# Optimization experiments

Hardware: AMD Instinct MI355X
Metric: run time of the kernel (lower is better)

Reference implementation:

```python
import jax, jax.numpy as jnp
import numpy as np

K = 8          # num groups
SIZE = 250     # state/hidden size (h1 = h2 = 250)
M = 576        # flattened input size (24x24)
B = 2048       # batch
HA = 100       # attention hidden
EPS = 1e-5


def _ln(x, g, b):
    mu = jnp.mean(x, axis=-1, keepdims=True)
    v = jnp.mean(jnp.square(x - mu), axis=-1, keepdims=True)
    return (x - mu) * jax.lax.rsqrt(v + EPS) * g + b


def setup_inputs() -> dict:
    key = jax.random.key(0)
    ks = jax.random.split(key, 10)
    def w(k, shape):
        return jax.random.normal(k, shape, jnp.float32) / np.sqrt(shape[0]).astype(np.float32)
    inp = {
        "x": jax.random.normal(ks[0], (B * K, M), jnp.float32),
        "state": jax.random.normal(ks[1], (B * K, SIZE), jnp.float32),
        # encoder: Linear(SIZE,250) + ReLU + LN(250)
        "enc_W": w(ks[2], (SIZE, 250)), "enc_b": jnp.zeros((250,), jnp.float32),
        "enc_g": jnp.ones((250,), jnp.float32), "enc_bt": jnp.zeros((250,), jnp.float32),
        # core: Linear(500,250) + ReLU + LN(250)
        "core_W": w(ks[3], (500, 250)), "core_b": jnp.zeros((250,), jnp.float32),
        "core_g": jnp.ones((250,), jnp.float32), "core_bt": jnp.zeros((250,), jnp.float32),
        # context: Linear(250,250) + ReLU + LN(250)
        "ctx_W": w(ks[4], (250, 250)), "ctx_b": jnp.zeros((250,), jnp.float32),
        "ctx_g": jnp.ones((250,), jnp.float32), "ctx_bt": jnp.zeros((250,), jnp.float32),
        # attention: Linear(250,100)+Tanh+LN(100)+Linear(100,1)+Sigmoid
        "att_W1": w(ks[5], (250, HA)), "att_b1": jnp.zeros((HA,), jnp.float32),
        "att_g": jnp.ones((HA,), jnp.float32), "att_bt": jnp.zeros((HA,), jnp.float32),
        "att_W2": w(ks[6], (HA, 1)), "att_b2": jnp.zeros((1,), jnp.float32),
        # output: Linear(250 + 250 + M, SIZE)
        "out_W": w(ks[7], (250 + 250 + M, SIZE)), "out_b": jnp.zeros((SIZE,), jnp.float32),
    }
    return inp


def reference(x, state, enc_W, enc_b, enc_g, enc_bt, core_W, core_b, core_g, core_bt,
              ctx_W, ctx_b, ctx_g, ctx_bt, att_W1, att_b1, att_g, att_bt,
              att_W2, att_b2, out_W, out_b):
    bk = state.shape[0]
    b = bk // K
    h1 = 250
    # 0-1. encode state -> [B*K, h1]
    s1 = _ln(jax.nn.relu(state @ enc_W + enc_b), enc_g, enc_bt)
    s1r = s1.reshape(b, K, h1)
    # 2-3. focus / context pairs via static gather index [K, K-1]
    idx = np.array([[j for j in range(K) if j != i] for i in range(K)], np.int32)
    cs = s1r[:, idx]                                    # [b, K, K-1, h1]
    fs = jnp.broadcast_to(s1r[:, :, None, :], cs.shape)  # [b, K, K-1, h1]
    # 4. concat pairs -> [b*K*(K-1), 2*h1]
    concat = jnp.concatenate([fs, cs], axis=-1).reshape(b * K * (K - 1), 2 * h1)
    # 5. core MLP
    core_out = _ln(jax.nn.relu(concat @ core_W + core_b), core_g, core_bt)
    # context MLP
    context_out = _ln(jax.nn.relu(core_out @ ctx_W + ctx_b), ctx_g, ctx_bt)
    # attention scalar per pair
    att_h = _ln(jnp.tanh(core_out @ att_W1 + att_b1), att_g, att_bt)
    att = jax.nn.sigmoid(att_h @ att_W2 + att_b2)        # [b*K*(K-1), 1]
    # 6-7. attention-weighted sum over K-1 context effects -> [B*K, h2]
    effect_sum = jnp.sum(context_out.reshape(bk, K - 1, h1) * att.reshape(bk, K - 1, 1), axis=1)
    # 8. decode
    total = jnp.concatenate([s1, effect_sum, x], axis=1)  # [B*K, h1+h2+M]
    new_state = total @ out_W + out_b                     # [B*K, SIZE]
    return new_state
```

## Files before the change

kernel.cpp:

```cpp
#include <hip/hip_runtime.h>
#include <math.h>

#define KK 8
#define H 250
#define MDIM 576
#define NB 2048
#define HA 100
#define ROWS (NB*KK)
#define PQS 512
#define KP 1088
#define EFS 258
#define EPS 1e-5f

typedef unsigned short ushort_t;
typedef short short8 __attribute__((ext_vector_type(8)));
typedef unsigned short us8 __attribute__((ext_vector_type(8)));
typedef unsigned short us4 __attribute__((ext_vector_type(4)));
typedef unsigned short us2 __attribute__((ext_vector_type(2)));
typedef float f32x4 __attribute__((ext_vector_type(4)));

template<int CTRL>
__device__ __forceinline__ float dpp_add_f32(float x) {
    const int s = __builtin_amdgcn_update_dpp(
        0, __builtin_bit_cast(int, x), CTRL, 0xF, 0xF, true);
    return x + __builtin_bit_cast(float, s);
}
__device__ __forceinline__ float wave_sum_dpp(float x) {
    x = dpp_add_f32<0x111>(x);
    x = dpp_add_f32<0x112>(x);
    x = dpp_add_f32<0x114>(x);
    x = dpp_add_f32<0x118>(x);
    x = dpp_add_f32<0x142>(x);
    x = dpp_add_f32<0x143>(x);
    return __builtin_bit_cast(float, __builtin_amdgcn_readlane(
        __builtin_bit_cast(int, x), 63));
}
__device__ __forceinline__ float bfly16_sum(float x) {
    x = dpp_add_f32<0xB1>(x);
    x = dpp_add_f32<0x4E>(x);
    x = dpp_add_f32<0x141>(x);
    x = dpp_add_f32<0x140>(x);
    return x;
}

__device__ __forceinline__ void async_copy16(const void* g, void* l) {
    __builtin_amdgcn_global_load_lds(
        (const __attribute__((address_space(1))) void*)g,
        (__attribute__((address_space(3))) void*)l, 16, 0, 0);
}

__device__ __forceinline__ ushort_t f2bf(float v) {
    union { float f; unsigned int u; } c; c.f = v;
    unsigned int x = c.u;
    x += 0x7fff + ((x >> 16) & 1);
    return (ushort_t)(x >> 16);
}
__device__ __forceinline__ float bf2f(ushort_t v) {
    union { unsigned int u; float f; } c; c.u = ((unsigned int)v) << 16;
    return c.f;
}
__device__ __forceinline__ float ftanh(float x) {
    const float e = __expf(2.f * x);
    return 1.f - 2.f * __builtin_amdgcn_rcpf(e + 1.f);
}
__device__ __forceinline__ float fsigmoid(float x) {
    return __builtin_amdgcn_rcpf(1.f + __expf(-x));
}

__global__ __launch_bounds__(256) void k_prep(
    const float* __restrict__ out_W, const float* __restrict__ core_W,
    const float* __restrict__ ctx_W, const float* __restrict__ att_W1,
    const float* __restrict__ enc_W, const float* __restrict__ state,
    const float* __restrict__ x,
    ushort_t* __restrict__ Wt, ushort_t* __restrict__ Wpq,
    ushort_t* __restrict__ Wca, ushort_t* __restrict__ Wenc,
    ushort_t* __restrict__ Sb, ushort_t* __restrict__ Abuf)
{
    const int b = blockIdx.x, t = threadIdx.x;
    if (b < 256) {
        const int n = b;
        for (int k = t; k < KP; k += 256) {
            const float v = (n < H && k < 1076) ? out_W[(size_t)k * H + n] : 0.f;
            Wt[(size_t)n * KP + k] = f2bf(v);
        }
    } else if (b < 768) {
        const int n = b - 256, k = t;
        float v = 0.f;
        if (k < H) {
            if (n < H)                    v = core_W[(size_t)k * H + n];
            else if (n >= 256 && n < 506) v = core_W[(size_t)(H + k) * H + (n - 256)];
        }
        Wpq[(size_t)n * 256 + k] = f2bf(v);
    } else if (b < 1152) {
        const int n = b - 768, k = t;
        float v = 0.f;
        if (k < H) {
            if (n < H)           v = ctx_W[(size_t)k * H + n];
            else if (n < H + HA) v = att_W1[(size_t)k * HA + (n - H)];
        }
        Wca[(size_t)n * 256 + k] = f2bf(v);
    } else if (b < 1408) {
        const int n = b - 1152, k = t;
        const float v = (n < H && k < H) ? enc_W[(size_t)k * H + n] : 0.f;
        Wenc[(size_t)n * 256 + k] = f2bf(v);
    } else if (b < 2432) {
        const int r0 = (b - 1408) * 16;
        for (int idx = t; idx < 16 * 256; idx += 256) {
            const int r = r0 + (idx >> 8), k = idx & 255;
            const float v = (k < H) ? state[(size_t)r * H + k] : 0.f;
            Sb[(size_t)r * 256 + k] = f2bf(v);
        }
    } else {
        const int row = b - 2432;
        for (int c = 500 + t; c < KP; c += 256) {
            const float v = (c < 500 + MDIM) ? x[(size_t)row * MDIM + (c - 500)] : 0.f;
            Abuf[(size_t)row * KP + c] = f2bf(v);
        }
    }
}

template<int NT>
__global__ __launch_bounds__(512, NT == 8 ? 2 : 4) void k_gemm_nres(
    const ushort_t* __restrict__ A, int lda,
    const ushort_t* __restrict__ B, int ldb,
    void* __restrict__ Cp, int ldc,
    const float* __restrict__ bias,
    int ksteps, int nlim, int bf16out)
{
    constexpr int NROWS = NT * 64;
    __shared__ __align__(16) ushort_t As[64 * 32];
    __shared__ __align__(16) ushort_t Bs[NROWS * 32];
    const int tid = threadIdx.x, lane = tid & 63, wave = tid >> 6;
    const int wm = wave >> 2, wn = wave & 3;
    const int R0 = (int)blockIdx.x * 64;

    const int ar = tid >> 2, acb = tid & 3;
    const bool aon = tid < 256;
    const int acl = acb ^ ((ar >> 1) & 3);
    const ushort_t* gA = A + (size_t)(R0 + ar) * lda + acl * 8;

    const int q = lane >> 4, fr = lane & 15;

    f32x4 acc[2][NT] = {};
    for (int ks = 0; ks < ksteps; ++ks) {
        const int k0 = ks * 32;
        if (aon) async_copy16(gA + k0, &As[tid * 8]);
#pragma unroll
        for (int it = 0; it < NT / 2; ++it) {
            const int ci  = it * 512 + tid;
            const int rb  = ci >> 2, cb2 = ci & 3;
            const int clb = cb2 ^ ((rb >> 1) & 3);
            async_copy16(B + (size_t)rb * ldb + k0 + clb * 8, &Bs[ci * 8]);
        }
        __syncthreads();
        short8 a[2];
#pragma unroll
        for (int ms = 0; ms < 2; ++ms) {
            const int row = wm * 32 + ms * 16 + fr;
            a[ms] = *(const short8*)&As[(row * 4 + (q ^ ((row >> 1) & 3))) * 8];
        }
#pragma unroll
        for (int nt = 0; nt < NT; ++nt) {
            const int n = wn * (NT * 16) + nt * 16 + fr;
            const short8 b = *(const short8*)&Bs[(n * 4 + (q ^ ((n >> 1) & 3))) * 8];
#pragma unroll
            for (int ms = 0; ms < 2; ++ms)
                acc[ms][nt] = __builtin_amdgcn_mfma_f32_16x16x32_bf16(
                    a[ms], b, acc[ms][nt], 0, 0, 0);
        }
        __syncthreads();
    }

#pragma unroll
    for (int ms = 0; ms < 2; ++ms)
#pragma unroll
        for (int nt = 0; nt < NT; ++nt) {
            const int col = wn * (NT * 16) + nt * 16 + fr;
            if (col >= nlim) continue;
            const float bv = bias ? bias[col] : 0.f;
#pragma unroll
            for (int reg = 0; reg < 4; ++reg) {
                const int row = R0 + wm * 32 + ms * 16 + q * 4 + reg;
                const float v = acc[ms][nt][reg] + bv;
                if (bf16out) ((ushort_t*)Cp)[(size_t)row * ldc + col] = f2bf(v);
                else         ((float*)Cp)[(size_t)row * ldc + col] = v;
            }
        }
}

__global__ __launch_bounds__(256) void k_lnenc(const ushort_t* __restrict__ Epre,
    const float* __restrict__ eb, const float* __restrict__ eg,
    const float* __restrict__ ebt, ushort_t* __restrict__ Abuf)
{
    const int wave = threadIdx.x >> 6, lane = threadIdx.x & 63;
    const int row = blockIdx.x * 4 + wave;
    const int c0 = 4 * lane;

    const us4 v = *(const us4*)&Epre[(size_t)row * 256 + c0];
    float y[4]; float sm = 0.f, sq = 0.f;
#pragma unroll
    for (int t = 0; t < 4; ++t) {
        const int cc = c0 + t;
        float z = 0.f;
        if (cc < H) z = fmaxf(bf2f(v[t]) + eb[cc], 0.f);
        y[t] = z; sm += z; sq += z * z;
    }
    sm = wave_sum_dpp(sm);
    sq = wave_sum_dpp(sq);
    const float mu = sm * (1.f / H);
    const float rs = __builtin_amdgcn_rsqf(sq * (1.f / H) - mu * mu + EPS);
    ushort_t o[4];
#pragma unroll
    for (int t = 0; t < 4; ++t) {
        const int cc = c0 + t;
        o[t] = (cc < H) ? f2bf((y[t] - mu) * rs * eg[cc] + ebt[cc]) : (ushort_t)0;
    }
    ushort_t* dst = Abuf + (size_t)row * KP + c0;
    if (c0 + 3 < H) { *(us4*)dst = (us4){o[0], o[1], o[2], o[3]}; }
    else {
        if (c0 + 1 < H) *(us2*)dst = (us2){o[0], o[1]};
    }
}

__global__ __launch_bounds__(512, 2) void k_fuse(
    const ushort_t* __restrict__ PQb,
    const ushort_t* __restrict__ Wca,
    const float* __restrict__ core_b, const float* __restrict__ core_g,
    const float* __restrict__ core_bt,
    const float* __restrict__ ctx_b, const float* __restrict__ ctx_g,
    const float* __restrict__ ctx_bt,
    const float* __restrict__ att_b1, const float* __restrict__ att_g,
    const float* __restrict__ att_bt,
    const float* __restrict__ attW2, const float* __restrict__ att_b2,
    ushort_t* __restrict__ Abuf)
{
    __shared__ __align__(16) ushort_t As[32 * 256];
    __shared__ __align__(16) ushort_t Bs[384 * 32];
    __shared__ __align__(16) float red[32][36];
    __shared__ __align__(16) float effacc[32 * EFS];
    __shared__ float scal[32];
    __shared__ float sS0[32], sS1[32];
    __shared__ float swred[4][2];

    const int tid = threadIdx.x, lane = tid & 63, wave = tid >> 6;
    const int wm = wave >> 2, wn = wave & 3;
    const int q = lane >> 4, fr = lane & 15;
    const int g0 = (int)blockIdx.x * 32;

    bool eC[6], eA[6];
    float b_[6], gw[6];
    float psgw = 0.f, psbw = 0.f;
#pragma unroll
    for (int nt = 0; nt < 6; ++nt) {
        const int col = wn * 96 + nt * 16 + fr;
        eC[nt] = col < H;
        eA[nt] = (col >= H) && (col < H + HA);
        if (eC[nt]) {
            b_[nt] = ctx_b[col]; gw[nt] = 0.f;
        } else if (eA[nt]) {
            const int ca = col - H;
            b_[nt] = att_b1[ca];
            const float ga = att_g[ca], w2 = attW2[ca];
            gw[nt] = ga * w2;
            psgw += gw[nt]; psbw += att_bt[ca] * w2;
        } else {
            b_[nt] = gw[nt] = 0.f;
        }
    }
    psgw = bfly16_sum(psgw); psbw = bfly16_sum(psbw);
    if (lane == 0) { swred[wn][0] = psgw; swred[wn][1] = psbw; }
    for (int i = tid; i < 32 * EFS; i += 512) effacc[i] = 0.f;
    if (wave == 0 && lane < 32) { sS0[lane] = 0.f; sS1[lane] = 0.f; }
    __syncthreads();
    const float sgw = swred[0][0] + swred[1][0] + swred[2][0] + swred[3][0];
    const float ab2 = att_b2[0] +
        (swred[0][1] + swred[1][1] + swred[2][1] + swred[3][1]);

    const int cL = lane * 4;
    float cb4[4], cg4[4], cbt4[4]; bool vl4[4];
#pragma unroll
    for (int t = 0; t < 4; ++t) {
        vl4[t] = (cL + t) < H;
        cb4[t] = cg4[t] = cbt4[t] = 0.f;
        if (vl4[t]) { cb4[t] = core_b[cL + t]; cg4[t] = core_g[cL + t];
                      cbt4[t] = core_bt[cL + t]; }
    }

    const int arow = wm * 16 + fr;
    const int abase = arow * 256;
    const int arsw = arow & 7;

    for (int jj = 0; jj < 7; ++jj) {
#pragma unroll
        for (int pass = 0; pass < 4; ++pass) {
            const int r = pass * 8 + wave;
            const int ir = r & 7;
            const int j = jj + (jj >= ir ? 1 : 0);
            const us4 pu = *(const us4*)&PQb[(size_t)(g0 + r) * PQS + cL];
            const us4 qu = *(const us4*)&PQb[
                (size_t)(g0 + (r & ~7) + j) * PQS + 256 + cL];
            float z[4]; float sm = 0.f, sq = 0.f;
#pragma unroll
            for (int t = 0; t < 4; ++t) {
                float zz = 0.f;
                if (vl4[t]) zz = fmaxf(bf2f(pu[t]) + bf2f(qu[t]) + cb4[t], 0.f);
                z[t] = zz; sm += zz; sq = fmaf(zz, zz, sq);
            }
            sm = wave_sum_dpp(sm);
            sq = wave_sum_dpp(sq);
            const float mu = sm * (1.f / H);
            const float rs = __builtin_amdgcn_rsqf(sq * (1.f / H) - mu * mu + EPS);
            us4 o;
#pragma unroll
            for (int t = 0; t < 4; ++t)
                o[t] = vl4[t] ? f2bf((z[t] - mu) * rs * cg4[t] + cbt4[t])
                              : (ushort_t)0;
            const int p = (((lane >> 1) ^ (r & 7)) << 1) | (lane & 1);
            *(us4*)&As[r * 256 + p * 4] = o;
        }

        f32x4 acc[6] = {};
        for (int ks = 0; ks < 8; ++ks) {
#pragma unroll
            for (int it = 0; it < 3; ++it) {
                const int ci  = it * 512 + tid;
                const int rb  = ci >> 2, cb2 = ci & 3;
                const int clb = cb2 ^ ((rb >> 1) & 3);
                async_copy16(Wca + (size_t)rb * 256 + ks * 32 + clb * 8, &Bs[ci * 8]);
            }
            __syncthreads();
            const short8 a = *(const short8*)&As[abase + ((ks * 4 + q) ^ arsw) * 8];
#pragma unroll
            for (int nt = 0; nt < 6; ++nt) {
                const int n = wn * 96 + nt * 16 + fr;
                const short8 b = *(const short8*)&Bs[(n * 4 + (q ^ ((n >> 1) & 3))) * 8];
                acc[nt] = __builtin_amdgcn_mfma_f32_16x16x32_bf16(a, b, acc[nt], 0, 0, 0);
            }
            __syncthreads();
        }

        float smc[4] = {}, sqc[4] = {}, sma[4] = {}, sqa[4] = {}, szgw[4] = {};
#pragma unroll
        for (int nt = 0; nt < 6; ++nt) {
#pragma unroll
            for (int reg = 0; reg < 4; ++reg) {
                const float val = acc[nt][reg] + b_[nt];
                if (eC[nt]) {
                    const float zz = fmaxf(val, 0.f);
                    acc[nt][reg] = zz;
                    smc[reg] += zz; sqc[reg] = fmaf(zz, zz, sqc[reg]);
                } else if (eA[nt]) {
                    const float za = ftanh(val);
                    sma[reg] += za; sqa[reg] = fmaf(za, za, sqa[reg]);
                    szgw[reg] = fmaf(za, gw[nt], szgw[reg]);
                }
            }
        }
#pragma unroll
        for (int reg = 0; reg < 4; ++reg) {
            smc[reg]  = bfly16_sum(smc[reg]);
            sqc[reg]  = bfly16_sum(sqc[reg]);
            sma[reg]  = bfly16_sum(sma[reg]);
            sqa[reg]  = bfly16_sum(sqa[reg]);
            szgw[reg] = bfly16_sum(szgw[reg]);
        }
        if (fr == 0) {
#pragma unroll
            for (int reg = 0; reg < 4; ++reg) {
                const int row = wm * 16 + q * 4 + reg;
                *(f32x4*)&red[row][wn * 8] =
                    (f32x4){smc[reg], sqc[reg], sma[reg], sqa[reg]};
                red[row][wn * 8 + 4] = szgw[reg];
            }
        }
        __syncthreads();
        if (wave == 0 && lane < 32) {
            const int rr = lane;
            float s0 = 0.f, s1 = 0.f, s2 = 0.f, s3 = 0.f, s4 = 0.f;
#pragma unroll
            for (int w2 = 0; w2 < 4; ++w2) {
                const f32x4 v = *(const f32x4*)&red[rr][w2 * 8];
                s0 += v[0]; s1 += v[1]; s2 += v[2]; s3 += v[3];
                s4 += red[rr][w2 * 8 + 4];
            }
            const float muC = s0 * (1.f / H);
            const float rsC = __builtin_amdgcn_rsqf(s1 * (1.f / H) - muC * muC + EPS);
            const float muA = s2 * (1.f / HA);
            const float rsA = __builtin_amdgcn_rsqf(s3 * (1.f / HA) - muA * muA + EPS);
            const float dot = rsA * (s4 - muA * sgw) + ab2;
            const float ag  = fsigmoid(dot);
            const float cj  = ag * rsC;
            scal[rr] = cj;
            sS0[rr] += ag;
            sS1[rr] = fmaf(cj, muC, sS1[rr]);
        }
        __syncthreads();
#pragma unroll
        for (int reg = 0; reg < 4; ++reg) {
            const int row = wm * 16 + q * 4 + reg;
            const float cj = scal[row];
#pragma unroll
            for (int nt = 0; nt < 6; ++nt) {
                if (!eC[nt]) continue;
                const int col = wn * 96 + nt * 16 + fr;
                const int idx = row * EFS + col;
                effacc[idx] = fmaf(cj, acc[nt][reg], effacc[idx]);
            }
        }
    }

#pragma unroll
    for (int nt = 0; nt < 6; ++nt) {
        const int col = wn * 96 + nt * 16 + fr;
        if (col >= H) continue;
        const float gc = ctx_g[col], bc = ctx_bt[col];
#pragma unroll
        for (int reg = 0; reg < 4; ++reg) {
            const int row = wm * 16 + q * 4 + reg;
            const float a4 = effacc[row * EFS + col];
            const float o = gc * (a4 - sS1[row]) + bc * sS0[row];
            Abuf[(size_t)(g0 + row) * KP + H + col] = f2bf(o);
        }
    }
}

extern "C" void kernel_launch(void* const* d_in, const int* in_sizes, int n_in,
                              void* d_out, int out_size, void* d_ws, size_t ws_size,
                              hipStream_t stream)
{
    const float* x      = (const float*)d_in[0];
    const float* state  = (const float*)d_in[1];
    const float* enc_W  = (const float*)d_in[2];
    const float* enc_b  = (const float*)d_in[3];
    const float* enc_g  = (const float*)d_in[4];
    const float* enc_bt = (const float*)d_in[5];
    const float* core_W = (const float*)d_in[6];
    const float* core_b = (const float*)d_in[7];
    const float* core_g = (const float*)d_in[8];
    const float* core_bt= (const float*)d_in[9];
    const float* ctx_W  = (const float*)d_in[10];
    const float* ctx_b  = (const float*)d_in[11];
    const float* ctx_g  = (const float*)d_in[12];
    const float* ctx_bt = (const float*)d_in[13];
    const float* att_W1 = (const float*)d_in[14];
    const float* att_b1 = (const float*)d_in[15];
    const float* att_g  = (const float*)d_in[16];
    const float* att_bt = (const float*)d_in[17];
    const float* att_W2 = (const float*)d_in[18];
    const float* att_b2 = (const float*)d_in[19];
    const float* out_W  = (const float*)d_in[20];
    const float* out_b  = (const float*)d_in[21];
    float* out = (float*)d_out;

    ushort_t* Abuf = (ushort_t*)d_ws;
    ushort_t* Wt   = Abuf + (size_t)ROWS * KP;
    ushort_t* Wpq  = Wt + (size_t)256 * KP;
    ushort_t* Wca  = Wpq + (size_t)512 * 256;
    ushort_t* Wenc = Wca + (size_t)384 * 256;
    ushort_t* Sb   = Wenc + (size_t)256 * 256;
    ushort_t* Epre = Sb + (size_t)ROWS * 256;
    ushort_t* PQb  = Epre + (size_t)ROWS * 256;

    k_prep  <<<2432 + ROWS, 256, 0, stream>>>(out_W, core_W, ctx_W, att_W1, enc_W,
                                              state, x, Wt, Wpq, Wca, Wenc, Sb, Abuf);
    k_gemm_nres<4><<<ROWS / 64, 512, 0, stream>>>(Sb, 256, Wenc, 256, Epre, 256,
                                                  nullptr, 8, 256, 1);
    k_lnenc <<<ROWS / 4, 256, 0, stream>>>(Epre, enc_b, enc_g, enc_bt, Abuf);
    k_gemm_nres<8><<<ROWS / 64, 512, 0, stream>>>(Abuf, KP, Wpq, 256, PQb, PQS,
                                                  nullptr, 8, 512, 1);
    k_fuse  <<<ROWS / 32, 512, 0, stream>>>(PQb, Wca,
                                            core_b, core_g, core_bt,
                                            ctx_b, ctx_g, ctx_bt,
                                            att_b1, att_g, att_bt,
                                            att_W2, att_b2, Abuf);
    k_gemm_nres<4><<<ROWS / 64, 512, 0, stream>>>(Abuf, KP, Wt, KP, out, H,
                                                  out_b, KP / 32, 250, 0);
}
```

Measured before the change: 348.2 us.

## Batch four pair-slices per weight load and keep effect sum in registers

The seven sequential j-iterations are regrouped into two sweeps of four and three slices. Each sweep builds a 128-row A tile in LDS, and every B-tile fetch of the combined context/attention weights is reused across up to four MFMA row-groups. That cuts weight reloads and block barriers per slice. The attention-weighted effect accumulator moves from an LDS array into registers, removing the LDS read-modify-write traffic and the zero-fill. The costs are a larger As buffer in LDS (128x256 bf16) and about 96 accumulator registers per lane, which could lower occupancy under the 512x2 launch bound.

```diff
diff --git a/kernel.cpp b/kernel.cpp
--- a/kernel.cpp
+++ b/kernel.cpp
@@ -9,7 +9,6 @@
 #define ROWS (NB*KK)
 #define PQS 512
 #define KP 1088
-#define EFS 258
 #define EPS 1e-5f
 
 typedef unsigned short ushort_t;
@@ -234,10 +233,9 @@
     const float* __restrict__ attW2, const float* __restrict__ att_b2,
     ushort_t* __restrict__ Abuf)
 {
-    __shared__ __align__(16) ushort_t As[32 * 256];
+    __shared__ __align__(16) ushort_t As[128 * 256];
     __shared__ __align__(16) ushort_t Bs[384 * 32];
     __shared__ __align__(16) float red[32][36];
-    __shared__ __align__(16) float effacc[32 * EFS];
     __shared__ float scal[32];
     __shared__ float sS0[32], sS1[32];
     __shared__ float swred[4][2];
@@ -269,7 +267,6 @@
     }
     psgw = bfly16_sum(psgw); psbw = bfly16_sum(psbw);
     if (lane == 0) { swred[wn][0] = psgw; swred[wn][1] = psbw; }
-    for (int i = tid; i < 32 * EFS; i += 512) effacc[i] = 0.f;
     if (wave == 0 && lane < 32) { sS0[lane] = 0.f; sS1[lane] = 0.f; }
     __syncthreads();
     const float sgw = swred[0][0] + swred[1][0] + swred[2][0] + swred[3][0];
@@ -287,18 +284,23 @@
     }
 
     const int arow = wm * 16 + fr;
-    const int abase = arow * 256;
     const int arsw = arow & 7;
 
-    for (int jj = 0; jj < 7; ++jj) {
-#pragma unroll
-        for (int pass = 0; pass < 4; ++pass) {
-            const int r = pass * 8 + wave;
-            const int ir = r & 7;
-            const int j = jj + (jj >= ir ? 1 : 0);
-            const us4 pu = *(const us4*)&PQb[(size_t)(g0 + r) * PQS + cL];
+    f32x4 A4[6] = {};
+
+    for (int sw = 0; sw < 2; ++sw) {
+        const int jb = sw * 4;
+        const int nj = 4 - sw;
+
+        for (int pass = 0; pass < nj * 4; ++pass) {
+            const int gr = pass * 8 + wave;
+            const int rl = gr & 31;
+            const int jj = jb + (gr >> 5);
+            const int ir = rl & 7;
+            const int j  = jj + (jj >= ir ? 1 : 0);
+            const us4 pu = *(const us4*)&PQb[(size_t)(g0 + rl) * PQS + cL];
             const us4 qu = *(const us4*)&PQb[
-                (size_t)(g0 + (r & ~7) + j) * PQS + 256 + cL];
+                (size_t)(g0 + (rl & ~7) + j) * PQS + 256 + cL];
             float z[4]; float sm = 0.f, sq = 0.f;
 #pragma unroll
             for (int t = 0; t < 4; ++t) {
@@ -315,11 +317,11 @@
             for (int t = 0; t < 4; ++t)
                 o[t] = vl4[t] ? f2bf((z[t] - mu) * rs * cg4[t] + cbt4[t])
                               : (ushort_t)0;
-            const int p = (((lane >> 1) ^ (r & 7)) << 1) | (lane & 1);
-            *(us4*)&As[r * 256 + p * 4] = o;
-        }
-
-        f32x4 acc[6] = {};
+            const int p = (((lane >> 1) ^ (rl & 7)) << 1) | (lane & 1);
+            *(us4*)&As[gr * 256 + p * 4] = o;
+        }
+
+        f32x4 acc[4][6] = {};
         for (int ks = 0; ks < 8; ++ks) {
 #pragma unroll
             for (int it = 0; it < 3; ++it) {
@@ -329,82 +331,93 @@
                 async_copy16(Wca + (size_t)rb * 256 + ks * 32 + clb * 8, &Bs[ci * 8]);
             }
             __syncthreads();
-            const short8 a = *(const short8*)&As[abase + ((ks * 4 + q) ^ arsw) * 8];
+            short8 bfr[6];
 #pragma unroll
             for (int nt = 0; nt < 6; ++nt) {
                 const int n = wn * 96 + nt * 16 + fr;
-                const short8 b = *(const short8*)&Bs[(n * 4 + (q ^ ((n >> 1) & 3))) * 8];
-                acc[nt] = __builtin_amdgcn_mfma_f32_16x16x32_bf16(a, b, acc[nt], 0, 0, 0);
+                bfr[nt] = *(const short8*)&Bs[(n * 4 + (q ^ ((n >> 1) & 3))) * 8];
+            }
+#pragma unroll
+            for (int u = 0; u < 4; ++u) {
+                if (u < nj) {
+                    const short8 a = *(const short8*)&As[
+                        (u * 32 + arow) * 256 + ((ks * 4 + q) ^ arsw) * 8];
+#pragma unroll
+                    for (int nt = 0; nt < 6; ++nt)
+                        acc[u][nt] = __builtin_amdgcn_mfma_f32_16x16x32_bf16(
+                            a, bfr[nt], acc[u][nt], 0, 0, 0);
+                }
             }
             __syncthreads();
         }
 
-        float smc[4] = {}, sqc[4] = {}, sma[4] = {}, sqa[4] = {}, szgw[4] = {};
-#pragma unroll
-        for (int nt = 0; nt < 6; ++nt) {
+#pragma unroll
+        for (int u = 0; u < 4; ++u) {
+            if (u >= nj) continue;
+            float smc[4] = {}, sqc[4] = {}, sma[4] = {}, sqa[4] = {}, szgw[4] = {};
+#pragma unroll
+            for (int nt = 0; nt < 6; ++nt) {
+#pragma unroll
+                for (int reg = 0; reg < 4; ++reg) {
+                    const float val = acc[u][nt][reg] + b_[nt];
+                    if (eC[nt]) {
+                        const float zz = fmaxf(val, 0.f);
+                        acc[u][nt][reg] = zz;
+                        smc[reg] += zz; sqc[reg] = fmaf(zz, zz, sqc[reg]);
+                    } else if (eA[nt]) {
+                        const float za = ftanh(val);
+                        sma[reg] += za; sqa[reg] = fmaf(za, za, sqa[reg]);
+                        szgw[reg] = fmaf(za, gw[nt], szgw[reg]);
+                    }
+                }
+            }
 #pragma unroll
             for (int reg = 0; reg < 4; ++reg) {
-                const float val = acc[nt][reg] + b_[nt];
-                if (eC[nt]) {
-                    const float zz = fmaxf(val, 0.f);
-                    acc[nt][reg] = zz;
-                    smc[reg] += zz; sqc[reg] = fmaf(zz, zz, sqc[reg]);
-                } else if (eA[nt]) {
-                    const float za = ftanh(val);
-                    sma[reg] += za; sqa[reg] = fmaf(za, za, sqa[reg]);
-                    szgw[reg] = fmaf(za, gw[nt], szgw[reg]);
+                smc[reg]  = bfly16_sum(smc[reg]);
+                sqc[reg]  = bfly16_sum(sqc[reg]);
+                sma[reg]  = bfly16_sum(sma[reg]);
+                sqa[reg]  = bfly16_sum(sqa[reg]);
+                szgw[reg] = bfly16_sum(szgw[reg]);
+            }
+            if (fr == 0) {
+#pragma unroll
+                for (int reg = 0; reg < 4; ++reg) {
+                    const int row = wm * 16 + q * 4 + reg;
+                    *(f32x4*)&red[row][wn * 8] =
+                        (f32x4){smc[reg], sqc[reg], sma[reg], sqa[reg]};
+                    red[row][wn * 8 + 4] = szgw[reg];
                 }
             }
-        }
-#pragma unroll
-        for (int reg = 0; reg < 4; ++reg) {
-            smc[reg]  = bfly16_sum(smc[reg]);
-            sqc[reg]  = bfly16_sum(sqc[reg]);
-            sma[reg]  = bfly16_sum(sma[reg]);
-            sqa[reg]  = bfly16_sum(sqa[reg]);
-            szgw[reg] = bfly16_sum(szgw[reg]);
-        }
-        if (fr == 0) {
+            __syncthreads();
+            if (wave == 0 && lane < 32) {
+                const int rr = lane;
+                float s0 = 0.f, s1 = 0.f, s2 = 0.f, s3 = 0.f, s4 = 0.f;
+#pragma unroll
+                for (int w2 = 0; w2 < 4; ++w2) {
+                    const f32x4 v = *(const f32x4*)&red[rr][w2 * 8];
+                    s0 += v[0]; s1 += v[1]; s2 += v[2]; s3 += v[3];
+                    s4 += red[rr][w2 * 8 + 4];
+                }
+                const float muC = s0 * (1.f / H);
+                const float rsC = __builtin_amdgcn_rsqf(s1 * (1.f / H) - muC * muC + EPS);
+                const float muA = s2 * (1.f / HA);
+                const float rsA = __builtin_amdgcn_rsqf(s3 * (1.f / HA) - muA * muA + EPS);
+                const float dot = rsA * (s4 - muA * sgw) + ab2;
+                const float ag  = fsigmoid(dot);
+                const float cj  = ag * rsC;
+                scal[rr] = cj;
+                sS0[rr] += ag;
+                sS1[rr] = fmaf(cj, muC, sS1[rr]);
+            }
+            __syncthreads();
 #pragma unroll
             for (int reg = 0; reg < 4; ++reg) {
                 const int row = wm * 16 + q * 4 + reg;
-                *(f32x4*)&red[row][wn * 8] =
-                    (f32x4){smc[reg], sqc[reg], sma[reg], sqa[reg]};
-                red[row][wn * 8 + 4] = szgw[reg];
-            }
-        }
-        __syncthreads();
-        if (wave == 0 && lane < 32) {
-            const int rr = lane;
-            float s0 = 0.f, s1 = 0.f, s2 = 0.f, s3 = 0.f, s4 = 0.f;
-#pragma unroll
-            for (int w2 = 0; w2 < 4; ++w2) {
-                const f32x4 v = *(const f32x4*)&red[rr][w2 * 8];
-                s0 += v[0]; s1 += v[1]; s2 += v[2]; s3 += v[3];
-                s4 += red[rr][w2 * 8 + 4];
-            }
-            const float muC = s0 * (1.f / H);
-            const float rsC = __builtin_amdgcn_rsqf(s1 * (1.f / H) - muC * muC + EPS);
-            const float muA = s2 * (1.f / HA);
-            const float rsA = __builtin_amdgcn_rsqf(s3 * (1.f / HA) - muA * muA + EPS);
-            const float dot = rsA * (s4 - muA * sgw) + ab2;
-            const float ag  = fsigmoid(dot);
-            const float cj  = ag * rsC;
-            scal[rr] = cj;
-            sS0[rr] += ag;
-            sS1[rr] = fmaf(cj, muC, sS1[rr]);
-        }
-        __syncthreads();
-#pragma unroll
-        for (int reg = 0; reg < 4; ++reg) {
-            const int row = wm * 16 + q * 4 + reg;
-            const float cj = scal[row];
-#pragma unroll
-            for (int nt = 0; nt < 6; ++nt) {
-                if (!eC[nt]) continue;
-                const int col = wn * 96 + nt * 16 + fr;
-                const int idx = row * EFS + col;
-                effacc[idx] = fmaf(cj, acc[nt][reg], effacc[idx]);
+                const float cj = scal[row];
+#pragma unroll
+                for (int nt = 0; nt < 6; ++nt)
+                    if (eC[nt])
+                        A4[nt][reg] = fmaf(cj, acc[u][nt][reg], A4[nt][reg]);
             }
         }
     }
@@ -417,8 +430,7 @@
 #pragma unroll
         for (int reg = 0; reg < 4; ++reg) {
             const int row = wm * 16 + q * 4 + reg;
-            const float a4 = effacc[row * EFS + col];
-            const float o = gc * (a4 - sS1[row]) + bc * sS0[row];
+            const float o = gc * (A4[nt][reg] - sS1[row]) + bc * sS0[row];
             Abuf[(size_t)(g0 + row) * KP + H + col] = f2bf(o);
         }
     }
```

Result: faster. 322.6 us (-7.3%).

## Split fused core/context kernel into core-LN pass plus pair-tiled context GEMM

Applied to the files above, without the earlier changes.

The fused kernel, which recomputed the core LayerNorm per pair inside a 7-iteration loop with a 32-row GEMM, is split into two kernels. The first writes all core outputs (B*K*7 rows) to a workspace buffer in bf16. The second runs a 64-row-tiled GEMM over flattened pair rows, grouping 9 groups (63 rows) per block, and accumulates the attention-weighted effect sums with LDS atomics. This trades an extra global round trip of about 58 MB of intermediate for better MFMA tile utilisation, fewer weight reloads per row and higher occupancy.

```diff
diff --git a/kernel.cpp b/kernel.cpp
--- a/kernel.cpp
+++ b/kernel.cpp
@@ -7,9 +7,10 @@
 #define NB 2048
 #define HA 100
 #define ROWS (NB*KK)
+#define PROWS (ROWS*7)
 #define PQS 512
 #define KP 1088
-#define EFS 258
+#define NGB 9
 #define EPS 1e-5f
 
 typedef unsigned short ushort_t;
@@ -222,11 +223,63 @@
     }
 }
 
-__global__ __launch_bounds__(512, 2) void k_fuse(
-    const ushort_t* __restrict__ PQb,
+__global__ __launch_bounds__(256) void k_core(const ushort_t* __restrict__ PQb,
+    const float* __restrict__ core_b, const float* __restrict__ core_g,
+    const float* __restrict__ core_bt, ushort_t* __restrict__ Co)
+{
+    const int wave = threadIdx.x >> 6, lane = threadIdx.x & 63;
+    const int g = blockIdx.x * 4 + wave;
+    const int i = g & 7;
+    const int c = lane * 4;
+
+    const us4 pu = *(const us4*)&PQb[(size_t)g * PQS + c];
+    us4 qu[7];
+#pragma unroll
+    for (int jj = 0; jj < 7; ++jj) {
+        const int j = jj + (jj >= i ? 1 : 0);
+        const int qr = (g & ~7) + j;
+        qu[jj] = *(const us4*)&PQb[(size_t)qr * PQS + 256 + c];
+    }
+    float pe[4], cb[4], cg[4], cbt[4]; bool vl[4];
+#pragma unroll
+    for (int t = 0; t < 4; ++t) {
+        vl[t]  = (c + t) < H;
+        pe[t]  = bf2f(pu[t]);
+        cb[t]  = vl[t] ? core_b[c + t]  : 0.f;
+        cg[t]  = vl[t] ? core_g[c + t]  : 0.f;
+        cbt[t] = vl[t] ? core_bt[c + t] : 0.f;
+    }
+    float z[7][4], red[7][2];
+#pragma unroll
+    for (int jj = 0; jj < 7; ++jj) {
+        float sm = 0.f, sq = 0.f;
+#pragma unroll
+        for (int t = 0; t < 4; ++t) {
+            const float zz = vl[t] ? fmaxf(pe[t] + bf2f(qu[jj][t]) + cb[t], 0.f) : 0.f;
+            z[jj][t] = zz; sm += zz; sq = fmaf(zz, zz, sq);
+        }
+        red[jj][0] = sm; red[jj][1] = sq;
+    }
+#pragma unroll
+    for (int jj = 0; jj < 7; ++jj) {
+        red[jj][0] = wave_sum_dpp(red[jj][0]);
+        red[jj][1] = wave_sum_dpp(red[jj][1]);
+    }
+#pragma unroll
+    for (int jj = 0; jj < 7; ++jj) {
+        const float mu = red[jj][0] * (1.f / H);
+        const float rs = __builtin_amdgcn_rsqf(red[jj][1] * (1.f / H) - mu * mu + EPS);
+        us4 o;
+#pragma unroll
+        for (int t = 0; t < 4; ++t)
+            o[t] = vl[t] ? f2bf((z[jj][t] - mu) * rs * cg[t] + cbt[t]) : (ushort_t)0;
+        *(us4*)&Co[((size_t)g * 7 + jj) * 256 + c] = o;
+    }
+}
+
+__global__ __launch_bounds__(512, 4) void k_cseff(
+    const ushort_t* __restrict__ Co,
     const ushort_t* __restrict__ Wca,
-    const float* __restrict__ core_b, const float* __restrict__ core_g,
-    const float* __restrict__ core_bt,
     const float* __restrict__ ctx_b, const float* __restrict__ ctx_g,
     const float* __restrict__ ctx_bt,
     const float* __restrict__ att_b1, const float* __restrict__ att_g,
@@ -234,18 +287,59 @@
     const float* __restrict__ attW2, const float* __restrict__ att_b2,
     ushort_t* __restrict__ Abuf)
 {
-    __shared__ __align__(16) ushort_t As[32 * 256];
+    __shared__ __align__(16) ushort_t As[64 * 32];
     __shared__ __align__(16) ushort_t Bs[384 * 32];
-    __shared__ __align__(16) float red[32][36];
-    __shared__ __align__(16) float effacc[32 * EFS];
-    __shared__ float scal[32];
-    __shared__ float sS0[32], sS1[32];
+    __shared__ __align__(16) float red[64][36];
+    __shared__ __align__(16) float scal[64][4];
+    __shared__ __align__(16) float effacc[NGB * 252];
+    __shared__ float sS0[NGB], sS1[NGB];
     __shared__ float swred[4][2];
 
     const int tid = threadIdx.x, lane = tid & 63, wave = tid >> 6;
     const int wm = wave >> 2, wn = wave & 3;
     const int q = lane >> 4, fr = lane & 15;
-    const int g0 = (int)blockIdx.x * 32;
+    const int gb0 = (int)blockIdx.x * NGB;
+    const int ngroups = min(NGB, ROWS - gb0);
+    const int nrows = ngroups * 7;
+    const int R0r = gb0 * 7;
+
+    for (int i = tid; i < NGB * 252; i += 512) effacc[i] = 0.f;
+
+    const int ar = tid >> 2, acb = tid & 3;
+    const bool aon = tid < 256;
+    const int acl = acb ^ ((ar >> 1) & 3);
+    const int arr = (ar < nrows) ? ar : (nrows - 1);
+    const ushort_t* gA = Co + (size_t)(R0r + arr) * 256 + acl * 8;
+
+    f32x4 acc[2][6] = {};
+    for (int ks = 0; ks < 8; ++ks) {
+        const int k0 = ks * 32;
+        if (aon) async_copy16(gA + k0, &As[tid * 8]);
+#pragma unroll
+        for (int it = 0; it < 3; ++it) {
+            const int ci  = it * 512 + tid;
+            const int rb  = ci >> 2, cb2 = ci & 3;
+            const int clb = cb2 ^ ((rb >> 1) & 3);
+            async_copy16(Wca + (size_t)rb * 256 + k0 + clb * 8, &Bs[ci * 8]);
+        }
+        __syncthreads();
+        short8 a[2];
+#pragma unroll
+        for (int ms = 0; ms < 2; ++ms) {
+            const int row = wm * 32 + ms * 16 + fr;
+            a[ms] = *(const short8*)&As[(row * 4 + (q ^ ((row >> 1) & 3))) * 8];
+        }
+#pragma unroll
+        for (int nt = 0; nt < 6; ++nt) {
+            const int n = wn * 96 + nt * 16 + fr;
+            const short8 b = *(const short8*)&Bs[(n * 4 + (q ^ ((n >> 1) & 3))) * 8];
+#pragma unroll
+            for (int ms = 0; ms < 2; ++ms)
+                acc[ms][nt] = __builtin_amdgcn_mfma_f32_16x16x32_bf16(
+                    a[ms], b, acc[ms][nt], 0, 0, 0);
+        }
+        __syncthreads();
+    }
 
     bool eC[6], eA[6];
     float b_[6], gw[6];
@@ -255,99 +349,29 @@
         const int col = wn * 96 + nt * 16 + fr;
         eC[nt] = col < H;
         eA[nt] = (col >= H) && (col < H + HA);
-        if (eC[nt]) {
-            b_[nt] = ctx_b[col]; gw[nt] = 0.f;
-        } else if (eA[nt]) {
+        if (eC[nt]) { b_[nt] = ctx_b[col]; gw[nt] = 0.f; }
+        else if (eA[nt]) {
             const int ca = col - H;
             b_[nt] = att_b1[ca];
-            const float ga = att_g[ca], w2 = attW2[ca];
-            gw[nt] = ga * w2;
+            const float w2 = attW2[ca];
+            gw[nt] = att_g[ca] * w2;
             psgw += gw[nt]; psbw += att_bt[ca] * w2;
-        } else {
-            b_[nt] = gw[nt] = 0.f;
-        }
+        } else { b_[nt] = gw[nt] = 0.f; }
     }
     psgw = bfly16_sum(psgw); psbw = bfly16_sum(psbw);
     if (lane == 0) { swred[wn][0] = psgw; swred[wn][1] = psbw; }
-    for (int i = tid; i < 32 * EFS; i += 512) effacc[i] = 0.f;
-    if (wave == 0 && lane < 32) { sS0[lane] = 0.f; sS1[lane] = 0.f; }
-    __syncthreads();
-    const float sgw = swred[0][0] + swred[1][0] + swred[2][0] + swred[3][0];
-    const float ab2 = att_b2[0] +
-        (swred[0][1] + swred[1][1] + swred[2][1] + swred[3][1]);
-
-    const int cL = lane * 4;
-    float cb4[4], cg4[4], cbt4[4]; bool vl4[4];
-#pragma unroll
-    for (int t = 0; t < 4; ++t) {
-        vl4[t] = (cL + t) < H;
-        cb4[t] = cg4[t] = cbt4[t] = 0.f;
-        if (vl4[t]) { cb4[t] = core_b[cL + t]; cg4[t] = core_g[cL + t];
-                      cbt4[t] = core_bt[cL + t]; }
-    }
-
-    const int arow = wm * 16 + fr;
-    const int abase = arow * 256;
-    const int arsw = arow & 7;
-
-    for (int jj = 0; jj < 7; ++jj) {
-#pragma unroll
-        for (int pass = 0; pass < 4; ++pass) {
-            const int r = pass * 8 + wave;
-            const int ir = r & 7;
-            const int j = jj + (jj >= ir ? 1 : 0);
-            const us4 pu = *(const us4*)&PQb[(size_t)(g0 + r) * PQS + cL];
-            const us4 qu = *(const us4*)&PQb[
-                (size_t)(g0 + (r & ~7) + j) * PQS + 256 + cL];
-            float z[4]; float sm = 0.f, sq = 0.f;
-#pragma unroll
-            for (int t = 0; t < 4; ++t) {
-                float zz = 0.f;
-                if (vl4[t]) zz = fmaxf(bf2f(pu[t]) + bf2f(qu[t]) + cb4[t], 0.f);
-                z[t] = zz; sm += zz; sq = fmaf(zz, zz, sq);
-            }
-            sm = wave_sum_dpp(sm);
-            sq = wave_sum_dpp(sq);
-            const float mu = sm * (1.f / H);
-            const float rs = __builtin_amdgcn_rsqf(sq * (1.f / H) - mu * mu + EPS);
-            us4 o;
-#pragma unroll
-            for (int t = 0; t < 4; ++t)
-                o[t] = vl4[t] ? f2bf((z[t] - mu) * rs * cg4[t] + cbt4[t])
-                              : (ushort_t)0;
-            const int p = (((lane >> 1) ^ (r & 7)) << 1) | (lane & 1);
-            *(us4*)&As[r * 256 + p * 4] = o;
-        }
-
-        f32x4 acc[6] = {};
-        for (int ks = 0; ks < 8; ++ks) {
-#pragma unroll
-            for (int it = 0; it < 3; ++it) {
-                const int ci  = it * 512 + tid;
-                const int rb  = ci >> 2, cb2 = ci & 3;
-                const int clb = cb2 ^ ((rb >> 1) & 3);
-                async_copy16(Wca + (size_t)rb * 256 + ks * 32 + clb * 8, &Bs[ci * 8]);
-            }
-            __syncthreads();
-            const short8 a = *(const short8*)&As[abase + ((ks * 4 + q) ^ arsw) * 8];
-#pragma unroll
-            for (int nt = 0; nt < 6; ++nt) {
-                const int n = wn * 96 + nt * 16 + fr;
-                const short8 b = *(const short8*)&Bs[(n * 4 + (q ^ ((n >> 1) & 3))) * 8];
-                acc[nt] = __builtin_amdgcn_mfma_f32_16x16x32_bf16(a, b, acc[nt], 0, 0, 0);
-            }
-            __syncthreads();
-        }
-
+
+#pragma unroll
+    for (int ms = 0; ms < 2; ++ms) {
         float smc[4] = {}, sqc[4] = {}, sma[4] = {}, sqa[4] = {}, szgw[4] = {};
 #pragma unroll
         for (int nt = 0; nt < 6; ++nt) {
 #pragma unroll
             for (int reg = 0; reg < 4; ++reg) {
-                const float val = acc[nt][reg] + b_[nt];
+                const float val = acc[ms][nt][reg] + b_[nt];
                 if (eC[nt]) {
                     const float zz = fmaxf(val, 0.f);
-                    acc[nt][reg] = zz;
+                    acc[ms][nt][reg] = zz;
                     smc[reg] += zz; sqc[reg] = fmaf(zz, zz, sqc[reg]);
                 } else if (eA[nt]) {
                     const float za = ftanh(val);
@@ -367,15 +391,22 @@
         if (fr == 0) {
 #pragma unroll
             for (int reg = 0; reg < 4; ++reg) {
-                const int row = wm * 16 + q * 4 + reg;
+                const int row = wm * 32 + ms * 16 + q * 4 + reg;
                 *(f32x4*)&red[row][wn * 8] =
                     (f32x4){smc[reg], sqc[reg], sma[reg], sqa[reg]};
                 red[row][wn * 8 + 4] = szgw[reg];
             }
         }
-        __syncthreads();
-        if (wave == 0 && lane < 32) {
-            const int rr = lane;
+    }
+    __syncthreads();
+
+    if (wave == 0) {
+        const float sgw = swred[0][0] + swred[1][0] + swred[2][0] + swred[3][0];
+        const float ab2 = att_b2[0] +
+            (swred[0][1] + swred[1][1] + swred[2][1] + swred[3][1]);
+        const int rr = lane;
+        float cj = 0.f, ag = 0.f, cm = 0.f;
+        if (rr < nrows) {
             float s0 = 0.f, s1 = 0.f, s2 = 0.f, s3 = 0.f, s4 = 0.f;
 #pragma unroll
             for (int w2 = 0; w2 < 4; ++w2) {
@@ -388,39 +419,47 @@
             const float muA = s2 * (1.f / HA);
             const float rsA = __builtin_amdgcn_rsqf(s3 * (1.f / HA) - muA * muA + EPS);
             const float dot = rsA * (s4 - muA * sgw) + ab2;
-            const float ag  = fsigmoid(dot);
-            const float cj  = ag * rsC;
-            scal[rr] = cj;
-            sS0[rr] += ag;
-            sS1[rr] = fmaf(cj, muC, sS1[rr]);
-        }
-        __syncthreads();
+            ag = fsigmoid(dot);
+            cj = ag * rsC;
+            cm = cj * muC;
+        }
+        *(f32x4*)&scal[rr][0] = (f32x4){cj, ag, cm, 0.f};
+    }
+    __syncthreads();
+
+#pragma unroll
+    for (int ms = 0; ms < 2; ++ms) {
 #pragma unroll
         for (int reg = 0; reg < 4; ++reg) {
-            const int row = wm * 16 + q * 4 + reg;
-            const float cj = scal[row];
+            const int row = wm * 32 + ms * 16 + q * 4 + reg;
+            if (row >= nrows) continue;
+            const float cj = scal[row][0];
+            const int gbase = (row / 7) * 252;
 #pragma unroll
             for (int nt = 0; nt < 6; ++nt) {
                 if (!eC[nt]) continue;
                 const int col = wn * 96 + nt * 16 + fr;
-                const int idx = row * EFS + col;
-                effacc[idx] = fmaf(cj, acc[nt][reg], effacc[idx]);
+                unsafeAtomicAdd(&effacc[gbase + col], cj * acc[ms][nt][reg]);
             }
         }
     }
-
-#pragma unroll
-    for (int nt = 0; nt < 6; ++nt) {
-        const int col = wn * 96 + nt * 16 + fr;
-        if (col >= H) continue;
-        const float gc = ctx_g[col], bc = ctx_bt[col];
-#pragma unroll
-        for (int reg = 0; reg < 4; ++reg) {
-            const int row = wm * 16 + q * 4 + reg;
-            const float a4 = effacc[row * EFS + col];
-            const float o = gc * (a4 - sS1[row]) + bc * sS0[row];
-            Abuf[(size_t)(g0 + row) * KP + H + col] = f2bf(o);
-        }
+    if (tid < NGB && tid < ngroups) {
+        float a0 = 0.f, a1 = 0.f;
+#pragma unroll
+        for (int j = 0; j < 7; ++j) {
+            a0 += scal[tid * 7 + j][1];
+            a1 += scal[tid * 7 + j][2];
+        }
+        sS0[tid] = a0; sS1[tid] = a1;
+    }
+    __syncthreads();
+
+    for (int i = tid; i < NGB * H; i += 512) {
+        const int gl = i / H, col = i - gl * H;
+        if (gl >= ngroups) break;
+        const float o = ctx_g[col] * (effacc[gl * 252 + col] - sS1[gl])
+                      + ctx_bt[col] * sS0[gl];
+        Abuf[(size_t)(gb0 + gl) * KP + H + col] = f2bf(o);
     }
 }
 
@@ -457,7 +496,8 @@
     ushort_t* Wpq  = Wt + (size_t)256 * KP;
     ushort_t* Wca  = Wpq + (size_t)512 * 256;
     ushort_t* Wenc = Wca + (size_t)384 * 256;
-    ushort_t* Sb   = Wenc + (size_t)256 * 256;
+    ushort_t* Co   = Wenc + (size_t)256 * 256;
+    ushort_t* Sb   = Co + (size_t)PROWS * 256;
     ushort_t* Epre = Sb + (size_t)ROWS * 256;
     ushort_t* PQb  = Epre + (size_t)ROWS * 256;
 
@@ -468,8 +508,8 @@
     k_lnenc <<<ROWS / 4, 256, 0, stream>>>(Epre, enc_b, enc_g, enc_bt, Abuf);
     k_gemm_nres<8><<<ROWS / 64, 512, 0, stream>>>(Abuf, KP, Wpq, 256, PQb, PQS,
                                                   nullptr, 8, 512, 1);
-    k_fuse  <<<ROWS / 32, 512, 0, stream>>>(PQb, Wca,
-                                            core_b, core_g, core_bt,
+    k_core  <<<ROWS / 4, 256, 0, stream>>>(PQb, core_b, core_g, core_bt, Co);
+    k_cseff <<<(ROWS + NGB - 1) / NGB, 512, 0, stream>>>(Co, Wca,
                                             ctx_b, ctx_g, ctx_bt,
                                             att_b1, att_g, att_bt,
                                             att_W2, att_b2, Abuf);
```

Result: slower. 447.8 us (+28.6%).
